# Optimization experiments

Hardware: AMD Instinct MI355X
Metric: run time of the kernel (lower is better)

The kernel has to match this reference:

```python
import jax, jax.numpy as jnp
from jax import lax
import numpy as np

EPS = 1e-5
TOPK_RATIO = 0.6

def _bn(y, gamma, beta, mean, var):
    # inference-mode BatchNorm3d over channel axis 1
    scale = gamma / jnp.sqrt(var + EPS)
    return (y - mean[None, :, None, None, None]) * scale[None, :, None, None, None] + beta[None, :, None, None, None]

def setup_inputs() -> dict:
    key = jax.random.key(0)
    ks = jax.random.split(key, 8)
    B, C, D, H, W = 4, 64, 16, 64, 64
    C8 = max(4, C // 8)  # bottleneck channels = 8
    x = jax.random.normal(ks[0], (B, C, D, H, W), dtype=jnp.float32)
    # depthwise conv weight, OIDHW with I=1 (groups=C), kernel (1,5,5)
    w_dw = jax.random.normal(ks[1], (C, 1, 1, 5, 5), dtype=jnp.float32) * 0.05
    bn1_gamma = jnp.ones((C,), jnp.float32)
    bn1_beta = jnp.zeros((C,), jnp.float32)
    bn1_mean = jax.random.normal(ks[2], (C,), jnp.float32) * 0.1
    bn1_var = jax.random.uniform(ks[3], (C,), jnp.float32, 0.5, 1.5)
    # pointwise 1x1x1 convs as matrices
    w_pw1 = jax.random.normal(ks[4], (C8, C), jnp.float32) * 0.05
    b_pw1 = jnp.zeros((C8,), jnp.float32)
    bn2_gamma = jnp.ones((C8,), jnp.float32)
    bn2_beta = jnp.zeros((C8,), jnp.float32)
    bn2_mean = jax.random.normal(ks[5], (C8,), jnp.float32) * 0.1
    bn2_var = jax.random.uniform(ks[6], (C8,), jnp.float32, 0.5, 1.5)
    w_pw2 = jax.random.normal(ks[7], (C, C8), jnp.float32) * 0.05
    b_pw2 = jnp.zeros((C,), jnp.float32)
    alpha = jnp.ones((), jnp.float32)
    return {"x": x, "w_dw": w_dw,
            "bn1_gamma": bn1_gamma, "bn1_beta": bn1_beta, "bn1_mean": bn1_mean, "bn1_var": bn1_var,
            "w_pw1": w_pw1, "b_pw1": b_pw1,
            "bn2_gamma": bn2_gamma, "bn2_beta": bn2_beta, "bn2_mean": bn2_mean, "bn2_var": bn2_var,
            "w_pw2": w_pw2, "b_pw2": b_pw2, "alpha": alpha}

def reference(x, w_dw, bn1_gamma, bn1_beta, bn1_mean, bn1_var,
              w_pw1, b_pw1, bn2_gamma, bn2_beta, bn2_mean, bn2_var,
              w_pw2, b_pw2, alpha):
    B, C, D, H, W = x.shape
    # branch1: depthwise conv3d (1,5,5), pad (0,2,2) + BN + SiLU
    y1 = lax.conv_general_dilated(
        x, w_dw, window_strides=(1, 1, 1),
        padding=((0, 0), (2, 2), (2, 2)),
        dimension_numbers=("NCDHW", "OIDHW", "NCDHW"),
        feature_group_count=C)
    y1 = jax.nn.silu(_bn(y1, bn1_gamma, bn1_beta, bn1_mean, bn1_var))
    # branch2: 1x1 conv -> BN -> SiLU -> 1x1 conv
    y2 = jnp.einsum("oc,bcdhw->bodhw", w_pw1, x) + b_pw1[None, :, None, None, None]
    y2 = jax.nn.silu(_bn(y2, bn2_gamma, bn2_beta, bn2_mean, bn2_var))
    y2 = jnp.einsum("oc,bcdhw->bodhw", w_pw2, y2) + b_pw2[None, :, None, None, None]
    attn = y1 * y2
    # channel-wise top-k threshold per spatial location
    k = max(1, int(TOPK_RATIO * C))
    attn_cl = jnp.moveaxis(attn, 1, -1)  # (B,D,H,W,C)
    thr = lax.top_k(attn_cl, k)[0][..., -1]  # k-th largest, (B,D,H,W)
    mask = (attn >= thr[:, None, :, :, :]).astype(attn.dtype)
    return x + alpha * (attn * mask)
```

## Files before the change

### kernel.cpp

```cpp
#include <hip/hip_runtime.h>

#define B  4
#define C  64
#define C8 8
#define DD 16
#define H  64
#define W  64
#define EPSV 1e-5f

__global__ __launch_bounds__(256) void dwconv_kernel(
    const float* __restrict__ x, const float* __restrict__ w_dw,
    const float* __restrict__ g1, const float* __restrict__ be1,
    const float* __restrict__ mu1, const float* __restrict__ va1,
    float* __restrict__ y1)
{
    const int blk = blockIdx.x;
    const int c = blk & 63;
    const int d = (blk >> 6) & 15;
    const int b = blk >> 10;

    float wk[25];
#pragma unroll
    for (int i = 0; i < 25; ++i) wk[i] = w_dw[c * 25 + i];
    const float scale = g1[c] * rsqrtf(va1[c] + EPSV);
    const float shift = be1[c] - mu1[c] * scale;

    const int tid = threadIdx.x;
    const int wq = (tid & 15) * 4;
    const long base = ((long)(b * C + c) * DD + d) * (H * W);

#pragma unroll
    for (int p = 0; p < 4; ++p) {
        const int h = (tid >> 4) + p * 16;
        float acc0 = 0.f, acc1 = 0.f, acc2 = 0.f, acc3 = 0.f;
#pragma unroll
        for (int j = 0; j < 5; ++j) {
            const int r = h + j - 2;
            if (r >= 0 && r < H) {
                const float4* rowp = (const float4*)(x + base + r * W);
                const int q = wq >> 2;
                float4 v0 = (wq >= 4)  ? rowp[q - 1] : make_float4(0.f, 0.f, 0.f, 0.f);
                float4 v1 = rowp[q];
                float4 v2 = (wq <= 56) ? rowp[q + 1] : make_float4(0.f, 0.f, 0.f, 0.f);
                float vals[12] = {v0.x, v0.y, v0.z, v0.w,
                                  v1.x, v1.y, v1.z, v1.w,
                                  v2.x, v2.y, v2.z, v2.w};
#pragma unroll
                for (int dw = 0; dw < 5; ++dw) {
                    const float kw = wk[j * 5 + dw];
                    acc0 += kw * vals[0 + 2 + dw];
                    acc1 += kw * vals[1 + 2 + dw];
                    acc2 += kw * vals[2 + 2 + dw];
                    acc3 += kw * vals[3 + 2 + dw];
                }
            }
        }
        float4 o;
        {
            float v = acc0 * scale + shift; o.x = v * (1.f / (1.f + __expf(-v)));
            v = acc1 * scale + shift;       o.y = v * (1.f / (1.f + __expf(-v)));
            v = acc2 * scale + shift;       o.z = v * (1.f / (1.f + __expf(-v)));
            v = acc3 * scale + shift;       o.w = v * (1.f / (1.f + __expf(-v)));
        }
        *(float4*)(y1 + base + h * W + wq) = o;
    }
}

__global__ __launch_bounds__(256) void fuse_kernel(
    const float* __restrict__ x, const float* __restrict__ y1,
    const float* __restrict__ w1, const float* __restrict__ b1,
    const float* __restrict__ g2, const float* __restrict__ be2,
    const float* __restrict__ mu2, const float* __restrict__ va2,
    const float* __restrict__ w2, const float* __restrict__ b2,
    const float* __restrict__ alphap, float* __restrict__ out)
{
    const int gid = blockIdx.x * 256 + threadIdx.x;
    const int b = gid >> 16;
    const int r = gid & 65535;
    const long base = (long)b * (C * 65536) + r;

    float s1[C8];
#pragma unroll
    for (int o = 0; o < C8; ++o) s1[o] = 0.f;
#pragma unroll
    for (int c = 0; c < C; ++c) {
        const float xc = x[base + (long)c * 65536];
#pragma unroll
        for (int o = 0; o < C8; ++o) s1[o] += w1[o * C + c] * xc;
    }
    float hh[C8];
#pragma unroll
    for (int o = 0; o < C8; ++o) {
        const float sc = g2[o] * rsqrtf(va2[o] + EPSV);
        const float v = (s1[o] + b1[o] - mu2[o]) * sc + be2[o];
        hh[o] = v * (1.f / (1.f + __expf(-v)));
    }

    float a[C], t[C];
#pragma unroll
    for (int c = 0; c < C; ++c) {
        float y2 = b2[c];
#pragma unroll
        for (int o = 0; o < C8; ++o) y2 += w2[c * C8 + o] * hh[o];
        const float av = y1[base + (long)c * 65536] * y2;
        a[c] = av;
        t[c] = av;
    }

#pragma unroll
    for (int k = 2; k <= 64; k <<= 1) {
#pragma unroll
        for (int j = k >> 1; j > 0; j >>= 1) {
#pragma unroll
            for (int i = 0; i < 64; ++i) {
                const int l = i ^ j;
                if (l > i) {
                    const float u = t[i], v = t[l];
                    const float mn = fminf(u, v), mx = fmaxf(u, v);
                    if ((i & k) == 0) { t[i] = mn; t[l] = mx; }
                    else              { t[i] = mx; t[l] = mn; }
                }
            }
        }
    }
    const float thr = t[26];
    const float alpha = alphap[0];

#pragma unroll
    for (int c = 0; c < C; ++c) {
        const float xc = x[base + (long)c * 65536];
        const float av = a[c];
        out[base + (long)c * 65536] = xc + ((av >= thr) ? alpha * av : 0.f);
    }
}

extern "C" void kernel_launch(void* const* d_in, const int* in_sizes, int n_in,
                              void* d_out, int out_size, void* d_ws, size_t ws_size,
                              hipStream_t stream) {
    const float* x    = (const float*)d_in[0];
    const float* w_dw = (const float*)d_in[1];
    const float* g1   = (const float*)d_in[2];
    const float* be1  = (const float*)d_in[3];
    const float* mu1  = (const float*)d_in[4];
    const float* va1  = (const float*)d_in[5];
    const float* w1   = (const float*)d_in[6];
    const float* b1   = (const float*)d_in[7];
    const float* g2   = (const float*)d_in[8];
    const float* be2  = (const float*)d_in[9];
    const float* mu2  = (const float*)d_in[10];
    const float* va2  = (const float*)d_in[11];
    const float* w2   = (const float*)d_in[12];
    const float* b2   = (const float*)d_in[13];
    const float* alp  = (const float*)d_in[14];
    float* out = (float*)d_out;
    float* y1  = (float*)d_ws;

    dwconv_kernel<<<B * DD * C, 256, 0, stream>>>(x, w_dw, g1, be1, mu1, va1, y1);
    fuse_kernel<<<(B * DD * H * W) / 256, 256, 0, stream>>>(
        x, y1, w1, b1, g2, be2, mu2, va2, w2, b2, alp, out);
}
```

Baseline: 259.3 us.

## Register-tile depthwise conv over 4x8 outputs and recompute attention to free registers

The depthwise conv kernel now has each thread compute a 4-row by 8-column output tile, with two channels per 256-thread block. Each loaded input row is reused across up to four output rows, which cuts redundant global and cache loads. In the fuse kernel the per-channel attention array is no longer kept alive across the sorting network. Instead y1 is re-read and y2 recomputed after the threshold is found, lowering register pressure at the cost of extra loads and FMAs. The larger conv tile increases per-thread register use and halves the grid size.

```diff
diff --git a/kernel.cpp b/kernel.cpp
--- a/kernel.cpp
+++ b/kernel.cpp
@@ -15,9 +15,12 @@
     float* __restrict__ y1)
 {
     const int blk = blockIdx.x;
-    const int c = blk & 63;
-    const int d = (blk >> 6) & 15;
-    const int b = blk >> 10;
+    const int half = threadIdx.x >> 7;
+    const int t = threadIdx.x & 127;
+    const int cpair = blk & 31;
+    const int d = (blk >> 5) & 15;
+    const int b = blk >> 9;
+    const int c = cpair * 2 + half;
 
     float wk[25];
 #pragma unroll
@@ -25,44 +28,58 @@
     const float scale = g1[c] * rsqrtf(va1[c] + EPSV);
     const float shift = be1[c] - mu1[c] * scale;
 
-    const int tid = threadIdx.x;
-    const int wq = (tid & 15) * 4;
+    const int w8 = (t & 7) * 8;
+    const int h4 = (t >> 3) * 4;
     const long base = ((long)(b * C + c) * DD + d) * (H * W);
 
+    float acc[4][8];
 #pragma unroll
-    for (int p = 0; p < 4; ++p) {
-        const int h = (tid >> 4) + p * 16;
-        float acc0 = 0.f, acc1 = 0.f, acc2 = 0.f, acc3 = 0.f;
+    for (int i = 0; i < 4; ++i)
 #pragma unroll
-        for (int j = 0; j < 5; ++j) {
-            const int r = h + j - 2;
-            if (r >= 0 && r < H) {
-                const float4* rowp = (const float4*)(x + base + r * W);
-                const int q = wq >> 2;
-                float4 v0 = (wq >= 4)  ? rowp[q - 1] : make_float4(0.f, 0.f, 0.f, 0.f);
-                float4 v1 = rowp[q];
-                float4 v2 = (wq <= 56) ? rowp[q + 1] : make_float4(0.f, 0.f, 0.f, 0.f);
-                float vals[12] = {v0.x, v0.y, v0.z, v0.w,
-                                  v1.x, v1.y, v1.z, v1.w,
-                                  v2.x, v2.y, v2.z, v2.w};
+        for (int ow = 0; ow < 8; ++ow) acc[i][ow] = 0.f;
+
 #pragma unroll
-                for (int dw = 0; dw < 5; ++dw) {
-                    const float kw = wk[j * 5 + dw];
-                    acc0 += kw * vals[0 + 2 + dw];
-                    acc1 += kw * vals[1 + 2 + dw];
-                    acc2 += kw * vals[2 + 2 + dw];
-                    acc3 += kw * vals[3 + 2 + dw];
+    for (int j = 0; j < 8; ++j) {
+        const int r = h4 + j - 2;
+        if (r >= 0 && r < H) {
+            const float4* rowp = (const float4*)(x + base + r * W);
+            const int q = w8 >> 2;
+            const float4 z = make_float4(0.f, 0.f, 0.f, 0.f);
+            float4 v0 = (w8 > 0)  ? rowp[q - 1] : z;
+            float4 v1 = rowp[q];
+            float4 v2 = rowp[q + 1];
+            float4 v3 = (w8 < 56) ? rowp[q + 2] : z;
+            float vals[16] = {v0.x, v0.y, v0.z, v0.w,
+                              v1.x, v1.y, v1.z, v1.w,
+                              v2.x, v2.y, v2.z, v2.w,
+                              v3.x, v3.y, v3.z, v3.w};
+#pragma unroll
+            for (int i = 0; i < 4; ++i) {
+                if (i <= j && (j - i) <= 4) {
+                    const int kr = j - i;
+#pragma unroll
+                    for (int dw = 0; dw < 5; ++dw) {
+                        const float kw = wk[kr * 5 + dw];
+#pragma unroll
+                        for (int ow = 0; ow < 8; ++ow)
+                            acc[i][ow] += kw * vals[ow + dw + 2];
+                    }
                 }
             }
         }
-        float4 o;
-        {
-            float v = acc0 * scale + shift; o.x = v * (1.f / (1.f + __expf(-v)));
-            v = acc1 * scale + shift;       o.y = v * (1.f / (1.f + __expf(-v)));
-            v = acc2 * scale + shift;       o.z = v * (1.f / (1.f + __expf(-v)));
-            v = acc3 * scale + shift;       o.w = v * (1.f / (1.f + __expf(-v)));
+    }
+
+#pragma unroll
+    for (int i = 0; i < 4; ++i) {
+        const int h = h4 + i;
+        float o[8];
+#pragma unroll
+        for (int ow = 0; ow < 8; ++ow) {
+            const float v = acc[i][ow] * scale + shift;
+            o[ow] = v * (1.f / (1.f + __expf(-v)));
         }
-        *(float4*)(y1 + base + h * W + wq) = o;
+        *(float4*)(y1 + base + h * W + w8)     = make_float4(o[0], o[1], o[2], o[3]);
+        *(float4*)(y1 + base + h * W + w8 + 4) = make_float4(o[4], o[5], o[6], o[7]);
     }
 }
 
@@ -96,15 +113,13 @@
         hh[o] = v * (1.f / (1.f + __expf(-v)));
     }
 
-    float a[C], t[C];
+    float t[C];
 #pragma unroll
     for (int c = 0; c < C; ++c) {
         float y2 = b2[c];
 #pragma unroll
         for (int o = 0; o < C8; ++o) y2 += w2[c * C8 + o] * hh[o];
-        const float av = y1[base + (long)c * 65536] * y2;
-        a[c] = av;
-        t[c] = av;
+        t[c] = y1[base + (long)c * 65536] * y2;
     }
 
 #pragma unroll
@@ -128,8 +143,11 @@
 
 #pragma unroll
     for (int c = 0; c < C; ++c) {
+        float y2 = b2[c];
+#pragma unroll
+        for (int o = 0; o < C8; ++o) y2 += w2[c * C8 + o] * hh[o];
+        const float av = y1[base + (long)c * 65536] * y2;
         const float xc = x[base + (long)c * 65536];
-        const float av = a[c];
         out[base + (long)c * 65536] = xc + ((av >= thr) ? alpha * av : 0.f);
     }
 }
@@ -155,7 +173,7 @@
     float* out = (float*)d_out;
     float* y1  = (float*)d_ws;
 
-    dwconv_kernel<<<B * DD * C, 256, 0, stream>>>(x, w_dw, g1, be1, mu1, va1, y1);
+    dwconv_kernel<<<(B * DD * C) / 2, 256, 0, stream>>>(x, w_dw, g1, be1, mu1, va1, y1);
     fuse_kernel<<<(B * DD * H * W) / 256, 256, 0, stream>>>(
         x, y1, w1, b1, g2, be2, mu2, va2, w2, b2, alp, out);
 }
```

Measured after the change: 237.8 us. 8.3% less time.

## Fuse depthwise conv into attention kernel via shared-memory y1 tile

Applied to the files above, without the earlier changes.

Merges the depthwise conv+BN+SiLU kernel into the pointwise/top-k kernel. Each block computes y1 for a 4-row tile across all 64 channels into 64KB of shared memory (skewed indexing to avoid bank conflicts), then each thread runs the channel-wise bitonic sort and writes output. This removes the y1 round trip through global memory and one launch. In exchange it uses a large shared-memory footprint and 64 accumulators per thread in the conv phase, which may lower occupancy, and it re-reads halo rows.

```diff
diff --git a/kernel.cpp b/kernel.cpp
--- a/kernel.cpp
+++ b/kernel.cpp
@@ -1,136 +1,151 @@
 #include <hip/hip_runtime.h>
 
-#define B  4
 #define C  64
 #define C8 8
-#define DD 16
-#define H  64
-#define W  64
 #define EPSV 1e-5f
 
-__global__ __launch_bounds__(256) void dwconv_kernel(
+__device__ __forceinline__ float silu_f(float v) {
+    return v * (1.f / (1.f + __expf(-v)));
+}
+
+__global__ __launch_bounds__(256) void fused_kernel(
     const float* __restrict__ x, const float* __restrict__ w_dw,
     const float* __restrict__ g1, const float* __restrict__ be1,
     const float* __restrict__ mu1, const float* __restrict__ va1,
-    float* __restrict__ y1)
-{
-    const int blk = blockIdx.x;
-    const int c = blk & 63;
-    const int d = (blk >> 6) & 15;
-    const int b = blk >> 10;
-
-    float wk[25];
-#pragma unroll
-    for (int i = 0; i < 25; ++i) wk[i] = w_dw[c * 25 + i];
-    const float scale = g1[c] * rsqrtf(va1[c] + EPSV);
-    const float shift = be1[c] - mu1[c] * scale;
-
-    const int tid = threadIdx.x;
-    const int wq = (tid & 15) * 4;
-    const long base = ((long)(b * C + c) * DD + d) * (H * W);
-
-#pragma unroll
-    for (int p = 0; p < 4; ++p) {
-        const int h = (tid >> 4) + p * 16;
-        float acc0 = 0.f, acc1 = 0.f, acc2 = 0.f, acc3 = 0.f;
-#pragma unroll
-        for (int j = 0; j < 5; ++j) {
-            const int r = h + j - 2;
-            if (r >= 0 && r < H) {
-                const float4* rowp = (const float4*)(x + base + r * W);
-                const int q = wq >> 2;
-                float4 v0 = (wq >= 4)  ? rowp[q - 1] : make_float4(0.f, 0.f, 0.f, 0.f);
-                float4 v1 = rowp[q];
-                float4 v2 = (wq <= 56) ? rowp[q + 1] : make_float4(0.f, 0.f, 0.f, 0.f);
-                float vals[12] = {v0.x, v0.y, v0.z, v0.w,
-                                  v1.x, v1.y, v1.z, v1.w,
-                                  v2.x, v2.y, v2.z, v2.w};
-#pragma unroll
-                for (int dw = 0; dw < 5; ++dw) {
-                    const float kw = wk[j * 5 + dw];
-                    acc0 += kw * vals[0 + 2 + dw];
-                    acc1 += kw * vals[1 + 2 + dw];
-                    acc2 += kw * vals[2 + 2 + dw];
-                    acc3 += kw * vals[3 + 2 + dw];
-                }
-            }
-        }
-        float4 o;
-        {
-            float v = acc0 * scale + shift; o.x = v * (1.f / (1.f + __expf(-v)));
-            v = acc1 * scale + shift;       o.y = v * (1.f / (1.f + __expf(-v)));
-            v = acc2 * scale + shift;       o.z = v * (1.f / (1.f + __expf(-v)));
-            v = acc3 * scale + shift;       o.w = v * (1.f / (1.f + __expf(-v)));
-        }
-        *(float4*)(y1 + base + h * W + wq) = o;
-    }
-}
-
-__global__ __launch_bounds__(256) void fuse_kernel(
-    const float* __restrict__ x, const float* __restrict__ y1,
     const float* __restrict__ w1, const float* __restrict__ b1,
     const float* __restrict__ g2, const float* __restrict__ be2,
     const float* __restrict__ mu2, const float* __restrict__ va2,
     const float* __restrict__ w2, const float* __restrict__ b2,
     const float* __restrict__ alphap, float* __restrict__ out)
 {
-    const int gid = blockIdx.x * 256 + threadIdx.x;
-    const int b = gid >> 16;
-    const int r = gid & 65535;
-    const long base = (long)b * (C * 65536) + r;
+    __shared__ float y1s[64 * 256];
 
-    float s1[C8];
+    const int blk = blockIdx.x;
+    const int hb = blk & 15;
+    const int d  = (blk >> 4) & 15;
+    const int b  = blk >> 8;
+    const int h0 = hb * 4;
+    const int tid = threadIdx.x;
+
+    {
+        const int c   = tid >> 2;
+        const int w16 = (tid & 3) * 16;
+        const int q   = w16 >> 2;
+
+        float wk[25];
 #pragma unroll
-    for (int o = 0; o < C8; ++o) s1[o] = 0.f;
+        for (int i = 0; i < 25; ++i) wk[i] = w_dw[c * 25 + i];
+        const float scale = g1[c] * rsqrtf(va1[c] + EPSV);
+        const float shift = be1[c] - mu1[c] * scale;
+        const long xbase = ((long)(b * C + c) * 16 + d) * 4096;
+
+        float acc[4][16];
 #pragma unroll
-    for (int c = 0; c < C; ++c) {
-        const float xc = x[base + (long)c * 65536];
+        for (int i = 0; i < 4; ++i)
 #pragma unroll
-        for (int o = 0; o < C8; ++o) s1[o] += w1[o * C + c] * xc;
-    }
-    float hh[C8];
-#pragma unroll
-    for (int o = 0; o < C8; ++o) {
-        const float sc = g2[o] * rsqrtf(va2[o] + EPSV);
-        const float v = (s1[o] + b1[o] - mu2[o]) * sc + be2[o];
-        hh[o] = v * (1.f / (1.f + __expf(-v)));
-    }
-
-    float a[C], t[C];
-#pragma unroll
-    for (int c = 0; c < C; ++c) {
-        float y2 = b2[c];
-#pragma unroll
-        for (int o = 0; o < C8; ++o) y2 += w2[c * C8 + o] * hh[o];
-        const float av = y1[base + (long)c * 65536] * y2;
-        a[c] = av;
-        t[c] = av;
-    }
+            for (int ow = 0; ow < 16; ++ow) acc[i][ow] = 0.f;
 
 #pragma unroll
-    for (int k = 2; k <= 64; k <<= 1) {
+        for (int j = 0; j < 8; ++j) {
+            const int r = h0 + j - 2;
+            if (r >= 0 && r < 64) {
+                const float4* rowp = (const float4*)(x + xbase + r * 64);
+                const float4 z = make_float4(0.f, 0.f, 0.f, 0.f);
+                float4 u0 = (q > 0)  ? rowp[q - 1] : z;
+                float4 u1 = rowp[q];
+                float4 u2 = rowp[q + 1];
+                float4 u3 = rowp[q + 2];
+                float4 u4 = rowp[q + 3];
+                float4 u5 = (q < 12) ? rowp[q + 4] : z;
+                float vals[24] = {u0.x,u0.y,u0.z,u0.w, u1.x,u1.y,u1.z,u1.w,
+                                  u2.x,u2.y,u2.z,u2.w, u3.x,u3.y,u3.z,u3.w,
+                                  u4.x,u4.y,u4.z,u4.w, u5.x,u5.y,u5.z,u5.w};
 #pragma unroll
-        for (int j = k >> 1; j > 0; j >>= 1) {
+                for (int i = 0; i < 4; ++i) {
+                    if (i <= j && (j - i) <= 4) {
+                        const int kr = j - i;
 #pragma unroll
-            for (int i = 0; i < 64; ++i) {
-                const int l = i ^ j;
-                if (l > i) {
-                    const float u = t[i], v = t[l];
-                    const float mn = fminf(u, v), mx = fmaxf(u, v);
-                    if ((i & k) == 0) { t[i] = mn; t[l] = mx; }
-                    else              { t[i] = mx; t[l] = mn; }
+                        for (int kc = 0; kc < 5; ++kc) {
+                            const float kw = wk[kr * 5 + kc];
+#pragma unroll
+                            for (int ow = 0; ow < 16; ++ow)
+                                acc[i][ow] += kw * vals[ow + kc + 2];
+                        }
+                    }
                 }
             }
         }
+#pragma unroll
+        for (int i = 0; i < 4; ++i)
+#pragma unroll
+            for (int ow = 0; ow < 16; ++ow) {
+                const int loc = i * 64 + w16 + ow;
+                y1s[loc * 64 + ((c + loc) & 63)] =
+                    silu_f(acc[i][ow] * scale + shift);
+            }
     }
-    const float thr = t[26];
-    const float alpha = alphap[0];
+    __syncthreads();
+
+    {
+        const int loc = tid;
+        const int h = h0 + (tid >> 6);
+        const int rg = d * 4096 + h * 64 + (tid & 63);
+        const float* xp = x + (long)b * (C * 65536) + rg;
+
+        float s1[C8];
+#pragma unroll
+        for (int o = 0; o < C8; ++o) s1[o] = 0.f;
+#pragma unroll
+        for (int c = 0; c < C; ++c) {
+            const float xc = xp[(long)c * 65536];
+#pragma unroll
+            for (int o = 0; o < C8; ++o) s1[o] += w1[o * C + c] * xc;
+        }
+        float hh[C8];
+#pragma unroll
+        for (int o = 0; o < C8; ++o) {
+            const float sc = g2[o] * rsqrtf(va2[o] + EPSV);
+            hh[o] = silu_f((s1[o] + b1[o] - mu2[o]) * sc + be2[o]);
+        }
+
+        float a[C], t[C];
+#pragma unroll
+        for (int c = 0; c < C; ++c) {
+            const float y1v = y1s[loc * 64 + ((c + loc) & 63)];
+            float y2 = b2[c];
+#pragma unroll
+            for (int o = 0; o < C8; ++o) y2 += w2[c * C8 + o] * hh[o];
+            const float av = y1v * y2;
+            a[c] = av;
+            t[c] = av;
+        }
 
 #pragma unroll
-    for (int c = 0; c < C; ++c) {
-        const float xc = x[base + (long)c * 65536];
-        const float av = a[c];
-        out[base + (long)c * 65536] = xc + ((av >= thr) ? alpha * av : 0.f);
+        for (int k = 2; k <= 64; k <<= 1) {
+#pragma unroll
+            for (int j = k >> 1; j > 0; j >>= 1) {
+#pragma unroll
+                for (int i = 0; i < 64; ++i) {
+                    const int l = i ^ j;
+                    if (l > i) {
+                        const float u = t[i], v = t[l];
+                        const float mn = fminf(u, v), mx = fmaxf(u, v);
+                        if ((i & k) == 0) { t[i] = mn; t[l] = mx; }
+                        else              { t[i] = mx; t[l] = mn; }
+                    }
+                }
+            }
+        }
+        const float thr = t[26];
+        const float alpha = alphap[0];
+        float* op = out + (long)b * (C * 65536) + rg;
+
+#pragma unroll
+        for (int c = 0; c < C; ++c) {
+            const float xc = xp[(long)c * 65536];
+            const float av = a[c];
+            op[(long)c * 65536] = xc + ((av >= thr) ? alpha * av : 0.f);
+        }
     }
 }
 
@@ -153,9 +168,7 @@
     const float* b2   = (const float*)d_in[13];
     const float* alp  = (const float*)d_in[14];
     float* out = (float*)d_out;
-    float* y1  = (float*)d_ws;
 
-    dwconv_kernel<<<B * DD * C, 256, 0, stream>>>(x, w_dw, g1, be1, mu1, va1, y1);
-    fuse_kernel<<<(B * DD * H * W) / 256, 256, 0, stream>>>(
-        x, y1, w1, b1, g2, be2, mu2, va2, w2, b2, alp, out);
+    fused_kernel<<<1024, 256, 0, stream>>>(
+        x, w_dw, g1, be1, mu1, va1, w1, b1, g2, be2, mu2, va2, w2, b2, alp, out);
 }
```

Result: faster. 226.7 us (-12.6%).
